# Performance work log

Measured on AMD Instinct MI355X. Metric: run time of the kernel, lower is better.

## Reference

```python
import jax, jax.numpy as jnp
import numpy as np

B, N, E = 64, 2048, 32768
F_IN, NHID, RULES = 256, 512, 128
RATIO = 0.5
K1 = int(np.ceil(RATIO * N)); K2 = int(np.ceil(RATIO * K1)); K3 = int(np.ceil(RATIO * K2))


def _gcn(x, src, dst, em, W, b):
    # GCNConv with self-loops and symmetric normalization; em is a float edge-validity mask.
    n = x.shape[0]
    h = x @ W  # [n, out]
    deg = jax.ops.segment_sum(em, dst, num_segments=n) + 1.0  # in-degree + self-loop
    dinv = jax.lax.rsqrt(deg)
    coef = dinv[src] * dinv[dst] * em  # [E]
    agg = jax.ops.segment_sum(h[src] * coef[:, None], dst, num_segments=n)
    return agg + h / deg[:, None] + b  # second term = self-loop with norm 1/deg


def _sag_pool(x, src, dst, em, Wg, bg, k):
    # SAGPooling: GCN scorer, per-graph top-k, scale kept nodes by tanh(score), filter+reindex edges.
    n = x.shape[0]
    score = _gcn(x, src, dst, em, Wg, bg)[:, 0]  # [n]
    vals, perm = jax.lax.top_k(score, k)
    xk = x[perm] * jnp.tanh(vals)[:, None]  # [k, F]
    newidx = jnp.full((n,), -1, dtype=src.dtype).at[perm].set(jnp.arange(k, dtype=src.dtype))
    ns, nd = newidx[src], newidx[dst]
    keep = em * (ns >= 0).astype(em.dtype) * (nd >= 0).astype(em.dtype)
    return xk, jnp.maximum(ns, 0), jnp.maximum(nd, 0), keep


_gcn_b = jax.vmap(_gcn, in_axes=(0, 0, 0, 0, None, None))
_pool_b = jax.vmap(_sag_pool, in_axes=(0, 0, 0, 0, None, None, None))


def setup_inputs() -> dict:
    key = jax.random.key(0)
    ks = jax.random.split(key, 16)
    def w(k, shape, fan_in):
        return jax.random.normal(k, shape, jnp.float32) * (1.0 / np.sqrt(fan_in))
    return {
        "x": jax.random.normal(ks[0], (B, N, F_IN), jnp.float32),
        "src": jax.random.randint(ks[1], (B, E), 0, N, jnp.int32),
        "dst": jax.random.randint(ks[2], (B, E), 0, N, jnp.int32),
        "W1": w(ks[3], (F_IN, NHID), F_IN), "b1": jnp.zeros((NHID,), jnp.float32),
        "Wp1": w(ks[4], (NHID, 1), NHID), "bp1": jnp.zeros((1,), jnp.float32),
        "W2": w(ks[5], (NHID, NHID), NHID), "b2": jnp.zeros((NHID,), jnp.float32),
        "Wp2": w(ks[6], (NHID, 1), NHID), "bp2": jnp.zeros((1,), jnp.float32),
        "W3": w(ks[7], (NHID, NHID), NHID), "b3": jnp.zeros((NHID,), jnp.float32),
        "Wp3": w(ks[8], (NHID, 1), NHID), "bp3": jnp.zeros((1,), jnp.float32),
        "lin1_W": w(ks[9], (2 * NHID, NHID), 2 * NHID), "lin1_b": jnp.zeros((NHID,), jnp.float32),
        "lin2_W": w(ks[10], (NHID, NHID // 2), NHID), "lin2_b": jnp.zeros((NHID // 2,), jnp.float32),
        "pi_W": w(ks[11], (NHID // 2, RULES), NHID // 2), "pi_b": jnp.zeros((RULES,), jnp.float32),
        "v_W": w(ks[12], (NHID // 2, 1), NHID // 2), "v_b": jnp.zeros((1,), jnp.float32),
    }


def reference(x, src, dst, W1, b1, Wp1, bp1, W2, b2, Wp2, bp2, W3, b3, Wp3, bp3,
              lin1_W, lin1_b, lin2_W, lin2_b, pi_W, pi_b, v_W, v_b):
    em = jnp.ones(src.shape, x.dtype)
    h = jax.nn.relu(_gcn_b(x, src, dst, em, W1, b1))
    h, s, d, em = _pool_b(h, src, dst, em, Wp1, bp1, K1)
    x1 = jnp.concatenate([h.max(axis=1), h.mean(axis=1)], axis=1)  # [B, 2*NHID]
    h = jax.nn.relu(_gcn_b(h, s, d, em, W2, b2))
    h, s, d, em = _pool_b(h, s, d, em, Wp2, bp2, K2)
    x2 = jnp.concatenate([h.max(axis=1), h.mean(axis=1)], axis=1)
    h = jax.nn.relu(_gcn_b(h, s, d, em, W3, b3))
    h, s, d, em = _pool_b(h, s, d, em, Wp3, bp3, K3)
    x3 = jnp.concatenate([h.max(axis=1), h.mean(axis=1)], axis=1)
    z = x1 + x2 + x3
    z = jax.nn.relu(z @ lin1_W + lin1_b)
    z = jax.nn.relu(z @ lin2_W + lin2_b)
    pi = jax.nn.log_softmax(z @ pi_W + pi_b, axis=1)
    v = jax.nn.relu(z @ v_W + v_b)
    return pi, v
```

## Files before the change

### kernel.cpp

```cpp
#include <hip/hip_runtime.h>
#include <math.h>
#include <cstdint>

#define B_   64
#define N_   2048
#define E_   32768
#define FIN  256
#define H_   512

typedef __bf16 bf16x8 __attribute__((ext_vector_type(8)));
typedef float  f32x4  __attribute__((ext_vector_type(4)));

__device__ __forceinline__ unsigned short f2bf(float f) {
  unsigned u = __float_as_uint(f);
  u += 0x7FFF + ((u >> 16) & 1);
  return (unsigned short)(u >> 16);
}
__device__ __forceinline__ unsigned pk2(float a, float b) {
  return (unsigned)f2bf(a) | ((unsigned)f2bf(b) << 16);
}
__device__ __forceinline__ float bflo(unsigned u) { return __uint_as_float(u << 16); }
__device__ __forceinline__ float bfhi(unsigned u) { return __uint_as_float(u & 0xFFFF0000u); }

__device__ __forceinline__ void accum8(float* acc, uint4 u, float c) {
  acc[0] += c * bflo(u.x); acc[1] += c * bfhi(u.x);
  acc[2] += c * bflo(u.y); acc[3] += c * bfhi(u.y);
  acc[4] += c * bflo(u.z); acc[5] += c * bfhi(u.z);
  acc[6] += c * bflo(u.w); acc[7] += c * bfhi(u.w);
}

__device__ __forceinline__ void glds16(const void* g, void* l) {
  __builtin_amdgcn_global_load_lds(
      (const __attribute__((address_space(1))) unsigned int*)g,
      (__attribute__((address_space(3))) unsigned int*)l, 16, 0, 0);
}

__global__ void xcvt_k(const float* __restrict__ x, unsigned short* __restrict__ xb) {
  int i = blockIdx.x * 256 + threadIdx.x;
  float4 f = reinterpret_cast<const float4*>(x)[i];
  uint2 o; o.x = pk2(f.x, f.y); o.y = pk2(f.z, f.w);
  reinterpret_cast<uint2*>(xb)[i] = o;
}

__global__ void wcvt_k(const float* __restrict__ W, unsigned short* __restrict__ Wt, int K) {
  int idx = blockIdx.x * 256 + threadIdx.x;
  int k = idx >> 9, n = idx & 511;
  Wt[n * K + k] = f2bf(W[idx]);
}

__global__ __launch_bounds__(256) void gemm_mfma(
    const unsigned short* __restrict__ Xb,
    const int* __restrict__ perm, const float* __restrict__ tanhv,
    const unsigned short* __restrict__ Wt, unsigned short* __restrict__ Y,
    int K, int kl2, int nsl2,
    const float* __restrict__ bias, const float* __restrict__ wp, float* __restrict__ hs) {
  __shared__ uint4 As[512];
  __shared__ uint4 Bs[512];
  const int tid = threadIdx.x;
  const int w = tid >> 6, L = tid & 63;
  const int bid = blockIdx.x;
  const int xcd = bid & 7;
  const int t = bid >> 3;
  const int colb = t & 3;
  const int strip = ((t >> 2) << 3) + xcd;
  const int m0 = strip * 128;
  const int n0 = colb * 128;
  const int e = L & 15, q = L >> 4;

  const int sw3 = (L >> 3) & 7;
  const int cA = (w * 64 + L) ^ sw3;
  const int rloc = cA >> 2;
  const int kcs = (cA & 3) * 8;

  f32x4 acc[4][4];
#pragma unroll
  for (int j = 0; j < 4; j++)
#pragma unroll
    for (int nn = 0; nn < 4; nn++) acc[j][nn] = (f32x4){0.f, 0.f, 0.f, 0.f};

  size_t asrc[2];
#pragma unroll
  for (int i = 0; i < 2; i++) {
    int g = m0 + i * 64 + rloc;
    size_t row;
    if (perm) {
      int b = g >> kl2;
      int node = perm[g];
      row = (size_t)(b << nsl2) + node;
    } else {
      row = (size_t)g;
    }
    asrc[i] = row * (size_t)K + kcs;
  }
  size_t bsrc[2];
#pragma unroll
  for (int i = 0; i < 2; i++) bsrc[i] = (size_t)(n0 + i * 64 + rloc) * K + kcs;

  const int fo = e * 4 + q;
  const int fosw = fo ^ (fo >> 3);

  for (int k0 = 0; k0 < K; k0 += 32) {
    glds16(Xb + asrc[0] + k0, &As[0 * 256 + w * 64]);
    glds16(Xb + asrc[1] + k0, &As[1 * 256 + w * 64]);
    glds16(Wt + bsrc[0] + k0, &Bs[0 * 256 + w * 64]);
    glds16(Wt + bsrc[1] + k0, &Bs[1 * 256 + w * 64]);
    __syncthreads();
    bf16x8 af[4], bfr[4];
#pragma unroll
    for (int j = 0; j < 4; j++) af[j]  = __builtin_bit_cast(bf16x8, As[((w & 1) * 4 + j) * 64 + fosw]);
#pragma unroll
    for (int j = 0; j < 4; j++) bfr[j] = __builtin_bit_cast(bf16x8, Bs[((w >> 1) * 4 + j) * 64 + fosw]);
#pragma unroll
    for (int j = 0; j < 4; j++)
#pragma unroll
      for (int nn = 0; nn < 4; nn++)
        acc[j][nn] = __builtin_amdgcn_mfma_f32_16x16x32_bf16(af[j], bfr[nn], acc[j][nn], 0, 0, 0);
    __syncthreads();
  }
  float bs[4], wsv[4];
#pragma unroll
  for (int nn = 0; nn < 4; nn++) {
    int coly = n0 + ((w >> 1) * 4 + nn) * 16 + e;
    bs[nn]  = bias ? bias[coly] : 0.f;
    wsv[nn] = wp ? wp[coly] : 0.f;
  }
#pragma unroll
  for (int j = 0; j < 4; j++) {
    int mt = (w & 1) * 4 + j;
#pragma unroll
    for (int r = 0; r < 4; r++) {
      int grow = m0 + mt * 16 + q * 4 + r;
      float t2 = tanhv ? tanhv[grow] : 1.0f;
      float p = 0.f;
#pragma unroll
      for (int nn = 0; nn < 4; nn++) {
        int coly = n0 + ((w >> 1) * 4 + nn) * 16 + e;
        float v = acc[j][nn][r] * t2;
        if (bias) v = fmaxf(v + bs[nn], 0.f);
        Y[(size_t)grow * 512 + coly] = f2bf(v);
        p += v * wsv[nn];
      }
      if (wp) {
        p += __shfl_xor(p, 1, 64); p += __shfl_xor(p, 2, 64);
        p += __shfl_xor(p, 4, 64); p += __shfl_xor(p, 8, 64);
        if ((L & 15) == 0) atomicAdd(&hs[grow], p);
      }
    }
  }
}

__global__ void count_k(const int* __restrict__ dst, int* __restrict__ cnt, int nl2) {
  int g = blockIdx.x * 256 + threadIdx.x;
  int d = dst[g];
  if (d < 0) return;
  int b = g >> 15;
  atomicAdd(&cnt[(b << nl2) + d], 1);
}

__global__ __launch_bounds__(256) void scan_k(const int* __restrict__ cnt,
                                              int* __restrict__ rowptr, int* __restrict__ cursor,
                                              float* __restrict__ deg, float* __restrict__ dinv, int n) {
  int b = blockIdx.x, tid = threadIdx.x;
  __shared__ int ls[2048];
  __shared__ int ch[256];
  int per = n >> 8;
  int base = tid * per;
  int s = 0;
  for (int i = 0; i < per; i++) { int v = cnt[b * n + base + i]; ls[base + i] = v; s += v; }
  ch[tid] = s;
  __syncthreads();
  for (int off = 1; off < 256; off <<= 1) {
    int v = (tid >= off) ? ch[tid - off] : 0;
    __syncthreads();
    ch[tid] += v;
    __syncthreads();
  }
  int run = (tid == 0) ? 0 : ch[tid - 1];
  for (int i = 0; i < per; i++) {
    int v = ls[base + i];
    rowptr[b * (n + 1) + base + i] = run;
    cursor[b * n + base + i] = run;
    float d = (float)(v + 1);
    deg[b * n + base + i] = d;
    dinv[b * n + base + i] = 1.0f / sqrtf(d);
    run += v;
  }
  if (tid == 255) rowptr[b * (n + 1) + n] = run;
}

__global__ void fill_k(const int* __restrict__ src, const int* __restrict__ dst,
                       const float* __restrict__ dinv, int* cursor, int* col,
                       float* ce, int nl2) {
  int g = blockIdx.x * 256 + threadIdx.x;
  int d = dst[g];
  if (d < 0) return;
  int b = g >> 15;
  int s = src[g];
  int pos = atomicAdd(&cursor[(b << nl2) + d], 1);
  col[(b << 15) + pos] = s;
  ce[(b << 15) + pos] = dinv[(b << nl2) + s] * dinv[(b << nl2) + d];
}

__global__ __launch_bounds__(256) void aggx_k(
    const unsigned short* __restrict__ X,
    const int* __restrict__ rowptr, const int* __restrict__ col,
    const float* __restrict__ ce, const float* __restrict__ deg,
    unsigned short* __restrict__ Xa) {
  const int w = threadIdx.x >> 6, L = threadIdx.x & 63;
  const int xcd = blockIdx.x & 7;
  const int slot = blockIdx.x >> 3;
  const int gslot = slot >> 9;
  const int v4 = slot & 511;
  const int b = (gslot << 3) + xcd;
  const int v = v4 * 4 + w;
  const int bbase = b << 11;
  const int vg = bbase + v;
  const int rb = b * (N_ + 1) + v;
  const int st = rowptr[rb], en = rowptr[rb + 1];
  const int* cb = col + (b << 15);
  const float* cee = ce + (b << 15);
  const int h = L >> 5, hl = L & 31;
  const unsigned short* Xb_ = X + (size_t)bbase * 256 + hl * 8;
  const int T = en - st + 1;
  const float selfc = 1.0f / deg[vg];
  float acc[8] = {0.f, 0.f, 0.f, 0.f, 0.f, 0.f, 0.f, 0.f};
  for (int t = h; t < T; t += 2) {
    bool isE = (t < T - 1);
    int s = isE ? cb[st + t] : v;
    float c = isE ? cee[st + t] : selfc;
    uint4 u = *(const uint4*)(Xb_ + (size_t)s * 256);
    accum8(acc, u, c);
  }
#pragma unroll
  for (int i = 0; i < 8; i++) acc[i] += __shfl_xor(acc[i], 32, 64);
  if (h == 0) {
    uint4 o;
    o.x = pk2(acc[0], acc[1]); o.y = pk2(acc[2], acc[3]);
    o.z = pk2(acc[4], acc[5]); o.w = pk2(acc[6], acc[7]);
    *(uint4*)(Xa + (size_t)vg * 256 + hl * 8) = o;
  }
}

template <int NL2>
__global__ __launch_bounds__(256) void agg_k(
    const unsigned short* __restrict__ H,
    const int* __restrict__ rowptr, const int* __restrict__ col,
    const float* __restrict__ ce, const float* __restrict__ deg,
    const float* __restrict__ bias, const float* __restrict__ wp,
    unsigned short* __restrict__ C, float* __restrict__ hs) {
  const int n = 1 << NL2;
  const int xcd = blockIdx.x & 7;
  const int slot = blockIdx.x >> 3;
  const int gslot = slot >> (NL2 - 2);
  const int v4 = slot & ((1 << (NL2 - 2)) - 1);
  const int b = (gslot << 3) + xcd;
  const int w = threadIdx.x >> 6, L = threadIdx.x & 63;
  const int v = v4 * 4 + w;
  const int bbase = b << NL2;
  const int vg = bbase + v;
  const int rb = b * (n + 1) + v;
  const int st = rowptr[rb], en = rowptr[rb + 1];
  const int* cb = col + (b << 15);
  const float* cee = ce + (b << 15);
  const unsigned short* Hb_ = H + (size_t)bbase * 512 + (size_t)L * 8;

  float acc[8] = {0.f, 0.f, 0.f, 0.f, 0.f, 0.f, 0.f, 0.f};
  int e2 = st;
  for (; e2 + 4 <= en; e2 += 4) {
    int s0 = cb[e2], s1 = cb[e2 + 1], s2 = cb[e2 + 2], s3 = cb[e2 + 3];
    float c0 = cee[e2], c1 = cee[e2 + 1], c2 = cee[e2 + 2], c3 = cee[e2 + 3];
    uint4 u0 = *(const uint4*)(Hb_ + (size_t)s0 * 512);
    uint4 u1 = *(const uint4*)(Hb_ + (size_t)s1 * 512);
    uint4 u2 = *(const uint4*)(Hb_ + (size_t)s2 * 512);
    uint4 u3 = *(const uint4*)(Hb_ + (size_t)s3 * 512);
    accum8(acc, u0, c0); accum8(acc, u1, c1);
    accum8(acc, u2, c2); accum8(acc, u3, c3);
  }
  for (; e2 < en; e2++) {
    int s = cb[e2];
    uint4 u = *(const uint4*)(Hb_ + (size_t)s * 512);
    accum8(acc, u, cee[e2]);
  }
  {
    float idg = 1.0f / deg[vg];
    uint4 u = *(const uint4*)(Hb_ + (size_t)v * 512);
    accum8(acc, u, idg);
  }
  float4 bLo = *(const float4*)(bias + L * 8);
  float4 bHi = *(const float4*)(bias + L * 8 + 4);
  acc[0] = fmaxf(acc[0] + bLo.x, 0.f); acc[1] = fmaxf(acc[1] + bLo.y, 0.f);
  acc[2] = fmaxf(acc[2] + bLo.z, 0.f); acc[3] = fmaxf(acc[3] + bLo.w, 0.f);
  acc[4] = fmaxf(acc[4] + bHi.x, 0.f); acc[5] = fmaxf(acc[5] + bHi.y, 0.f);
  acc[6] = fmaxf(acc[6] + bHi.z, 0.f); acc[7] = fmaxf(acc[7] + bHi.w, 0.f);
  uint4 o;
  o.x = pk2(acc[0], acc[1]); o.y = pk2(acc[2], acc[3]);
  o.z = pk2(acc[4], acc[5]); o.w = pk2(acc[6], acc[7]);
  *(uint4*)(C + (size_t)vg * 512 + L * 8) = o;
  float4 wLo = *(const float4*)(wp + L * 8);
  float4 wHi = *(const float4*)(wp + L * 8 + 4);
  float p = acc[0] * wLo.x + acc[1] * wLo.y + acc[2] * wLo.z + acc[3] * wLo.w
          + acc[4] * wHi.x + acc[5] * wHi.y + acc[6] * wHi.z + acc[7] * wHi.w;
#pragma unroll
  for (int off = 32; off > 0; off >>= 1) p += __shfl_down(p, off, 64);
  if (L == 0) hs[vg] = p;
}

__global__ void scoreagg_k(const float* __restrict__ hs, const int* __restrict__ rowptr,
                           const int* __restrict__ col, const float* __restrict__ ce,
                           const float* __restrict__ deg, const float* __restrict__ bp,
                           float* __restrict__ score, int nl2) {
  int idx = blockIdx.x * 256 + threadIdx.x;
  int n = 1 << nl2;
  int b = idx >> nl2, v = idx & (n - 1);
  int rb = b * (n + 1) + v;
  int st = rowptr[rb], en = rowptr[rb + 1];
  const int* cb = col + (b << 15);
  const float* cee = ce + (b << 15);
  int bbase = b << nl2;
  float acc = 0.f;
  int e = st;
  for (; e + 4 <= en; e += 4) {
    acc += hs[bbase + cb[e]] * cee[e] + hs[bbase + cb[e + 1]] * cee[e + 1]
         + hs[bbase + cb[e + 2]] * cee[e + 2] + hs[bbase + cb[e + 3]] * cee[e + 3];
  }
  for (; e < en; e++) acc += hs[bbase + cb[e]] * cee[e];
  score[idx] = acc + hs[idx] / deg[idx] + bp[0];
}

__global__ __launch_bounds__(1024) void topk_k(const float* __restrict__ score, int* __restrict__ perm,
                                               float* __restrict__ tanhv, int* __restrict__ newidx,
                                               int n, int k) {
  int b = blockIdx.x, tid = threadIdx.x;
  __shared__ float ss[2048];
  __shared__ int si[2048];
  for (int i = tid; i < n; i += 1024) { ss[i] = score[b * n + i]; si[i] = i; }
  __syncthreads();
  for (int size = 2; size <= n; size <<= 1) {
    for (int stride = size >> 1; stride > 0; stride >>= 1) {
      for (int i = tid; i < n; i += 1024) {
        int j = i ^ stride;
        if (j > i) {
          bool up = ((i & size) == 0);
          float fi = ss[i], fj = ss[j];
          int ii = si[i], ij = si[j];
          bool iBefore = (fi > fj) || (fi == fj && ii < ij);
          bool sw = up ? (!iBefore) : iBefore;
          if (sw) { ss[i] = fj; ss[j] = fi; si[i] = ij; si[j] = ii; }
        }
      }
      __syncthreads();
    }
  }
  for (int r = tid; r < n; r += 1024) newidx[b * n + si[r]] = (r < k) ? r : -1;
  for (int r = tid; r < k; r += 1024) { perm[b * k + r] = si[r]; tanhv[b * k + r] = tanhf(ss[r]); }
}

__global__ void reindex_count_k(const int* srcO, const int* dstO, const int* newidx,
                                int* srcN, int* dstN, int* cnt, int nl2new) {
  int g = blockIdx.x * 256 + threadIdx.x;
  int b = g >> 15;
  int dd = dstO[g];
  int sN = 0, dN = -1;
  if (dd >= 0) {
    int ns = newidx[(b << (nl2new + 1)) + srcO[g]];
    int nd = newidx[(b << (nl2new + 1)) + dd];
    if (ns >= 0 && nd >= 0) {
      sN = ns; dN = nd;
      atomicAdd(&cnt[(b << nl2new) + nd], 1);
    }
  }
  srcN[g] = sN; dstN[g] = dN;
}

__global__ __launch_bounds__(512) void statsp_k(const unsigned short* __restrict__ C,
    const int* __restrict__ perm, const float* __restrict__ tv,
    float* __restrict__ zp, int nsl2, int k, int kch) {
  int b = blockIdx.x, rg = blockIdx.y, f = threadIdx.x;
  int r0 = rg * kch;
  float mx = -1e30f, sm = 0.f;
#pragma unroll 4
  for (int r = r0; r < r0 + kch; r++) {
    int node = perm[b * k + r];
    float t = tv[b * k + r];
    float val = __uint_as_float((unsigned)C[((size_t)((b << nsl2) + node)) * 512 + f] << 16) * t;
    mx = fmaxf(mx, val); sm += val;
  }
  zp[(size_t)(b * 8 + rg) * 1024 + f] = mx;
  zp[(size_t)(b * 8 + rg) * 1024 + 512 + f] = sm;
}

__global__ __launch_bounds__(512) void statsr_k(const float* __restrict__ zp,
                                                float* __restrict__ z, int k) {
  int b = blockIdx.x, f = threadIdx.x;
  float mx = -1e30f, sm = 0.f;
#pragma unroll
  for (int g = 0; g < 8; g++) {
    mx = fmaxf(mx, zp[(size_t)(b * 8 + g) * 1024 + f]);
    sm += zp[(size_t)(b * 8 + g) * 1024 + 512 + f];
  }
  z[b * 1024 + f] += mx;
  z[b * 1024 + 512 + f] += sm / (float)k;
}

__global__ __launch_bounds__(256) void mlp_k(const float* __restrict__ z, const float* __restrict__ W1,
                                             const float* __restrict__ b1, const float* __restrict__ W2,
                                             const float* __restrict__ b2, const float* __restrict__ piW,
                                             const float* __restrict__ pib, const float* __restrict__ vW,
                                             const float* __restrict__ vb, float* __restrict__ out) {
  int b = blockIdx.x, tid = threadIdx.x;
  __shared__ float zr[1024];
  __shared__ float z1[512];
  __shared__ float z2[256];
  __shared__ float pl[128];
  __shared__ float red[2];
  for (int i = tid; i < 1024; i += 256) zr[i] = z[b * 1024 + i];
  __syncthreads();
  for (int o = tid; o < 512; o += 256) {
    float a = b1[o];
    for (int i = 0; i < 1024; i++) a += zr[i] * W1[i * 512 + o];
    z1[o] = fmaxf(a, 0.f);
  }
  __syncthreads();
  {
    int o = tid;
    float a = b2[o];
    for (int i = 0; i < 512; i++) a += z1[i] * W2[i * 256 + o];
    z2[o] = fmaxf(a, 0.f);
  }
  __syncthreads();
  if (tid < 128) {
    float a = pib[tid];
    for (int i = 0; i < 256; i++) a += z2[i] * piW[i * 128 + tid];
    pl[tid] = a;
  }
  __syncthreads();
  if (tid == 0) {
    float m = -1e30f;
    for (int i = 0; i < 128; i++) m = fmaxf(m, pl[i]);
    float se = 0.f;
    for (int i = 0; i < 128; i++) se += expf(pl[i] - m);
    red[0] = m; red[1] = logf(se);
    float a = vb[0];
    for (int i = 0; i < 256; i++) a += z2[i] * vW[i];
    out[B_ * 128 + b] = fmaxf(a, 0.f);
  }
  __syncthreads();
  if (tid < 128) out[b * 128 + tid] = pl[tid] - red[0] - red[1];
}

extern "C" void kernel_launch(void* const* d_in, const int* in_sizes, int n_in,
                              void* d_out, int out_size, void* d_ws, size_t ws_size,
                              hipStream_t stream) {
  const float* x    = (const float*)d_in[0];
  const int*   src0 = (const int*)d_in[1];
  const int*   dst0 = (const int*)d_in[2];
  const float* W1   = (const float*)d_in[3];
  const float* b1   = (const float*)d_in[4];
  const float* Wp1  = (const float*)d_in[5];
  const float* bp1  = (const float*)d_in[6];
  const float* W2   = (const float*)d_in[7];
  const float* b2   = (const float*)d_in[8];
  const float* Wp2  = (const float*)d_in[9];
  const float* bp2  = (const float*)d_in[10];
  const float* W3   = (const float*)d_in[11];
  const float* b3   = (const float*)d_in[12];
  const float* Wp3  = (const float*)d_in[13];
  const float* bp3  = (const float*)d_in[14];
  const float* l1W  = (const float*)d_in[15];
  const float* l1b  = (const float*)d_in[16];
  const float* l2W  = (const float*)d_in[17];
  const float* l2b  = (const float*)d_in[18];
  const float* piW  = (const float*)d_in[19];
  const float* pib  = (const float*)d_in[20];
  const float* vW   = (const float*)d_in[21];
  const float* vb   = (const float*)d_in[22];
  float* out = (float*)d_out;
  (void)in_sizes; (void)n_in; (void)out_size; (void)ws_size;

  unsigned short* Cb = (unsigned short*)d_in[0];

  char* base = (char*)d_ws;
  size_t off = 0;
  auto alloc = [&](size_t bytes) -> void* {
    void* r = base + off;
    off += (bytes + 255) & ~(size_t)255;
    return r;
  };
  unsigned short* Hb   = (unsigned short*)alloc((size_t)B_ * 1024 * H_ * 2);
  unsigned short* xb   = (unsigned short*)alloc((size_t)B_ * N_ * FIN * 2);
  unsigned short* Xa   = (unsigned short*)alloc((size_t)B_ * N_ * FIN * 2);
  unsigned short* W1t  = (unsigned short*)alloc((size_t)512 * 256 * 2);
  unsigned short* W2t  = (unsigned short*)alloc((size_t)512 * 512 * 2);
  unsigned short* W3t  = (unsigned short*)alloc((size_t)512 * 512 * 2);
  int*   srcA   = (int*)alloc((size_t)B_ * E_ * 4);
  int*   dstA   = (int*)alloc((size_t)B_ * E_ * 4);
  int*   col    = (int*)alloc((size_t)B_ * E_ * 4);
  float* coefE  = (float*)alloc((size_t)B_ * E_ * 4);
  int*   cnt    = (int*)alloc((size_t)B_ * N_ * 4);
  int*   cursor = (int*)alloc((size_t)B_ * N_ * 4);
  int*   rowptr = (int*)alloc((size_t)B_ * (N_ + 1) * 4);
  float* deg    = (float*)alloc((size_t)B_ * N_ * 4);
  float* dinv   = (float*)alloc((size_t)B_ * N_ * 4);
  float* hs     = (float*)alloc((size_t)B_ * N_ * 4);
  float* score  = (float*)alloc((size_t)B_ * N_ * 4);
  int*   newidx = (int*)alloc((size_t)B_ * N_ * 4);
  int*   perm   = (int*)alloc((size_t)B_ * 1024 * 4);
  float* tanhv  = (float*)alloc((size_t)B_ * 1024 * 4);
  float* zpart  = (float*)alloc((size_t)B_ * 8 * 1024 * 4);
  float* z      = (float*)alloc((size_t)B_ * 1024 * 4);

  const int EB = B_ * E_ / 256;

  xcvt_k<<<B_ * N_ * FIN / 4 / 256, 256, 0, stream>>>(x, xb);
  wcvt_k<<<256 * 512 / 256, 256, 0, stream>>>(W1, W1t, 256);
  wcvt_k<<<512 * 512 / 256, 256, 0, stream>>>(W2, W2t, 512);
  wcvt_k<<<512 * 512 / 256, 256, 0, stream>>>(W3, W3t, 512);
  hipMemsetAsync(z, 0, (size_t)B_ * 1024 * 4, stream);

  {
    hipMemsetAsync(cnt, 0, (size_t)B_ * 2048 * 4, stream);
    count_k<<<EB, 256, 0, stream>>>(dst0, cnt, 11);
    scan_k<<<B_, 256, 0, stream>>>(cnt, rowptr, cursor, deg, dinv, 2048);
    fill_k<<<EB, 256, 0, stream>>>(src0, dst0, dinv, cursor, col, coefE, 11);
    aggx_k<<<B_ * 2048 / 4, 256, 0, stream>>>(xb, rowptr, col, coefE, deg, Xa);
    hipMemsetAsync(hs, 0, (size_t)B_ * 2048 * 4, stream);
    gemm_mfma<<<B_ * 2048 / 128 * 4, 256, 0, stream>>>(
        Xa, nullptr, nullptr, W1t, Cb, 256, 0, 0, b1, Wp1, hs);
    scoreagg_k<<<B_ * 2048 / 256, 256, 0, stream>>>(hs, rowptr, col, coefE, deg, bp1, score, 11);
    topk_k<<<B_, 1024, 0, stream>>>(score, perm, tanhv, newidx, 2048, 1024);
    statsp_k<<<dim3(B_, 8), 512, 0, stream>>>(Cb, perm, tanhv, zpart, 11, 1024, 128);
    statsr_k<<<B_, 512, 0, stream>>>(zpart, z, 1024);
    hipMemsetAsync(cnt, 0, (size_t)B_ * 1024 * 4, stream);
    reindex_count_k<<<EB, 256, 0, stream>>>(src0, dst0, newidx, srcA, dstA, cnt, 10);
    scan_k<<<B_, 256, 0, stream>>>(cnt, rowptr, cursor, deg, dinv, 1024);
    fill_k<<<EB, 256, 0, stream>>>(srcA, dstA, dinv, cursor, col, coefE, 10);
  }
  {
    gemm_mfma<<<B_ * 1024 / 128 * 4, 256, 0, stream>>>(
        Cb, perm, tanhv, W2t, Hb, 512, 10, 11, nullptr, nullptr, nullptr);
    agg_k<10><<<B_ * 1024 / 4, 256, 0, stream>>>(Hb, rowptr, col, coefE, deg, b2, Wp2, Cb, hs);
    scoreagg_k<<<B_ * 1024 / 256, 256, 0, stream>>>(hs, rowptr, col, coefE, deg, bp2, score, 10);
    topk_k<<<B_, 1024, 0, stream>>>(score, perm, tanhv, newidx, 1024, 512);
    statsp_k<<<dim3(B_, 8), 512, 0, stream>>>(Cb, perm, tanhv, zpart, 10, 512, 64);
    statsr_k<<<B_, 512, 0, stream>>>(zpart, z, 512);
    hipMemsetAsync(cnt, 0, (size_t)B_ * 512 * 4, stream);
    reindex_count_k<<<EB, 256, 0, stream>>>(srcA, dstA, newidx, srcA, dstA, cnt, 9);
    scan_k<<<B_, 256, 0, stream>>>(cnt, rowptr, cursor, deg, dinv, 512);
    fill_k<<<EB, 256, 0, stream>>>(srcA, dstA, dinv, cursor, col, coefE, 9);
  }
  {
    gemm_mfma<<<B_ * 512 / 128 * 4, 256, 0, stream>>>(
        Cb, perm, tanhv, W3t, Hb, 512, 9, 10, nullptr, nullptr, nullptr);
    agg_k<9><<<B_ * 512 / 4, 256, 0, stream>>>(Hb, rowptr, col, coefE, deg, b3, Wp3, Cb, hs);
    scoreagg_k<<<B_ * 512 / 256, 256, 0, stream>>>(hs, rowptr, col, coefE, deg, bp3, score, 9);
    topk_k<<<B_, 1024, 0, stream>>>(score, perm, tanhv, newidx, 512, 256);
    statsp_k<<<dim3(B_, 8), 512, 0, stream>>>(Cb, perm, tanhv, zpart, 9, 256, 32);
    statsr_k<<<B_, 512, 0, stream>>>(zpart, z, 256);
  }

  mlp_k<<<B_, 256, 0, stream>>>(z, l1W, l1b, l2W, l2b, piW, pib, vW, vb, out);
}
```

Baseline: 1.104 ms.

## Widen GEMM tile to 128x256 with shuffle-packed vector stores and hardware bf16 pack

The MFMA GEMM tile grows from 128x128 to 128x256 outputs per block, so each wave holds a 4x8 accumulator grid and the A tile is reused across twice as many columns. Grid size is halved. The epilogue uses lane shuffles to pack neighbouring bf16 outputs into 8-byte stores instead of scalar 2-byte stores. On gfx950 the float-to-bf16 pack uses the native v_cvt_pk_bf16_f32 instruction. The trade-off is more registers and shared memory per block and fewer blocks, which may lower occupancy and wave parallelism on the smaller layer-3 GEMM.

New measurement: 1.256 ms. 1.14x slower.

```diff
diff --git a/kernel.cpp b/kernel.cpp
--- a/kernel.cpp
+++ b/kernel.cpp
@@ -17,7 +17,13 @@
   return (unsigned short)(u >> 16);
 }
 __device__ __forceinline__ unsigned pk2(float a, float b) {
+#if defined(__gfx950__)
+  unsigned r;
+  asm("v_cvt_pk_bf16_f32 %0, %1, %2" : "=v"(r) : "v"(a), "v"(b));
+  return r;
+#else
   return (unsigned)f2bf(a) | ((unsigned)f2bf(b) << 16);
+#endif
 }
 __device__ __forceinline__ float bflo(unsigned u) { return __uint_as_float(u << 16); }
 __device__ __forceinline__ float bfhi(unsigned u) { return __uint_as_float(u & 0xFFFF0000u); }
@@ -55,28 +61,28 @@
     int K, int kl2, int nsl2,
     const float* __restrict__ bias, const float* __restrict__ wp, float* __restrict__ hs) {
   __shared__ uint4 As[512];
-  __shared__ uint4 Bs[512];
+  __shared__ uint4 Bs[1024];
   const int tid = threadIdx.x;
   const int w = tid >> 6, L = tid & 63;
   const int bid = blockIdx.x;
   const int xcd = bid & 7;
   const int t = bid >> 3;
-  const int colb = t & 3;
-  const int strip = ((t >> 2) << 3) + xcd;
+  const int colb = t & 1;
+  const int strip = ((t >> 1) << 3) + xcd;
   const int m0 = strip * 128;
-  const int n0 = colb * 128;
   const int e = L & 15, q = L >> 4;
+  const int mh = w & 1, nh = w >> 1;
 
   const int sw3 = (L >> 3) & 7;
   const int cA = (w * 64 + L) ^ sw3;
   const int rloc = cA >> 2;
   const int kcs = (cA & 3) * 8;
 
-  f32x4 acc[4][4];
+  f32x4 acc[4][8];
 #pragma unroll
   for (int j = 0; j < 4; j++)
 #pragma unroll
-    for (int nn = 0; nn < 4; nn++) acc[j][nn] = (f32x4){0.f, 0.f, 0.f, 0.f};
+    for (int nn = 0; nn < 8; nn++) acc[j][nn] = (f32x4){0.f, 0.f, 0.f, 0.f};
 
   size_t asrc[2];
 #pragma unroll
@@ -92,9 +98,9 @@
     }
     asrc[i] = row * (size_t)K + kcs;
   }
-  size_t bsrc[2];
-#pragma unroll
-  for (int i = 0; i < 2; i++) bsrc[i] = (size_t)(n0 + i * 64 + rloc) * K + kcs;
+  size_t bsrc[4];
+#pragma unroll
+  for (int i = 0; i < 4; i++) bsrc[i] = (size_t)(colb * 256 + i * 64 + rloc) * K + kcs;
 
   const int fo = e * 4 + q;
   const int fosw = fo ^ (fo >> 3);
@@ -104,43 +110,69 @@
     glds16(Xb + asrc[1] + k0, &As[1 * 256 + w * 64]);
     glds16(Wt + bsrc[0] + k0, &Bs[0 * 256 + w * 64]);
     glds16(Wt + bsrc[1] + k0, &Bs[1 * 256 + w * 64]);
+    glds16(Wt + bsrc[2] + k0, &Bs[2 * 256 + w * 64]);
+    glds16(Wt + bsrc[3] + k0, &Bs[3 * 256 + w * 64]);
     __syncthreads();
-    bf16x8 af[4], bfr[4];
-#pragma unroll
-    for (int j = 0; j < 4; j++) af[j]  = __builtin_bit_cast(bf16x8, As[((w & 1) * 4 + j) * 64 + fosw]);
-#pragma unroll
-    for (int j = 0; j < 4; j++) bfr[j] = __builtin_bit_cast(bf16x8, Bs[((w >> 1) * 4 + j) * 64 + fosw]);
+    bf16x8 af[4], bfr[8];
 #pragma unroll
     for (int j = 0; j < 4; j++)
-#pragma unroll
-      for (int nn = 0; nn < 4; nn++)
+      af[j] = __builtin_bit_cast(bf16x8, As[mh * 256 + j * 64 + fosw]);
+#pragma unroll
+    for (int nn = 0; nn < 8; nn++)
+      bfr[nn] = __builtin_bit_cast(bf16x8, Bs[(nh * 2 + (nn >> 2)) * 256 + (nn & 3) * 64 + fosw]);
+#pragma unroll
+    for (int j = 0; j < 4; j++)
+#pragma unroll
+      for (int nn = 0; nn < 8; nn++)
         acc[j][nn] = __builtin_amdgcn_mfma_f32_16x16x32_bf16(af[j], bfr[nn], acc[j][nn], 0, 0, 0);
     __syncthreads();
   }
-  float bs[4], wsv[4];
-#pragma unroll
-  for (int nn = 0; nn < 4; nn++) {
-    int coly = n0 + ((w >> 1) * 4 + nn) * 16 + e;
+  const int colbase = colb * 256 + nh * 128;
+  float bs[8], wsv[8];
+#pragma unroll
+  for (int nn = 0; nn < 8; nn++) {
+    int coly = colbase + nn * 16 + e;
     bs[nn]  = bias ? bias[coly] : 0.f;
     wsv[nn] = wp ? wp[coly] : 0.f;
   }
 #pragma unroll
   for (int j = 0; j < 4; j++) {
-    int mt = (w & 1) * 4 + j;
 #pragma unroll
     for (int r = 0; r < 4; r++) {
-      int grow = m0 + mt * 16 + q * 4 + r;
+      int grow = m0 + (mh * 4 + j) * 16 + q * 4 + r;
       float t2 = tanhv ? tanhv[grow] : 1.0f;
-      float p = 0.f;
-#pragma unroll
-      for (int nn = 0; nn < 4; nn++) {
-        int coly = n0 + ((w >> 1) * 4 + nn) * 16 + e;
-        float v = acc[j][nn][r] * t2;
-        if (bias) v = fmaxf(v + bs[nn], 0.f);
-        Y[(size_t)grow * 512 + coly] = f2bf(v);
-        p += v * wsv[nn];
+      float v[8];
+#pragma unroll
+      for (int nn = 0; nn < 8; nn++) {
+        float val = acc[j][nn][r] * t2;
+        if (bias) val = fmaxf(val + bs[nn], 0.f);
+        v[nn] = val;
+      }
+      unsigned u[4];
+      const bool odd = (e & 1);
+#pragma unroll
+      for (int tt = 0; tt < 4; tt++) {
+        float a = v[2 * tt], b = v[2 * tt + 1];
+        float a2 = __shfl_xor(a, 1, 64);
+        float b2 = __shfl_xor(b, 1, 64);
+        u[tt] = odd ? pk2(b2, b) : pk2(a, a2);
+      }
+      unsigned short* Yr = Y + (size_t)grow * 512;
+#pragma unroll
+      for (int s = 0; s < 2; s++) {
+        unsigned ua = u[2 * s], ub = u[2 * s + 1];
+        unsigned ua2 = __shfl_xor(ua, 2, 64);
+        unsigned ub2 = __shfl_xor(ub, 2, 64);
+        uint2 wv;
+        if (e & 2) { wv.x = ub2; wv.y = ub; }
+        else       { wv.x = ua;  wv.y = ua2; }
+        int T = s * 4 + (e & 3);
+        *(uint2*)(Yr + colbase + T * 16 + (e & 12)) = wv;
       }
       if (wp) {
+        float p = 0.f;
+#pragma unroll
+        for (int nn = 0; nn < 8; nn++) p += v[nn] * wsv[nn];
         p += __shfl_xor(p, 1, 64); p += __shfl_xor(p, 2, 64);
         p += __shfl_xor(p, 4, 64); p += __shfl_xor(p, 8, 64);
         if ((L & 15) == 0) atomicAdd(&hs[grow], p);
@@ -524,7 +556,7 @@
     fill_k<<<EB, 256, 0, stream>>>(src0, dst0, dinv, cursor, col, coefE, 11);
     aggx_k<<<B_ * 2048 / 4, 256, 0, stream>>>(xb, rowptr, col, coefE, deg, Xa);
     hipMemsetAsync(hs, 0, (size_t)B_ * 2048 * 4, stream);
-    gemm_mfma<<<B_ * 2048 / 128 * 4, 256, 0, stream>>>(
+    gemm_mfma<<<B_ * 2048 / 128 * 2, 256, 0, stream>>>(
         Xa, nullptr, nullptr, W1t, Cb, 256, 0, 0, b1, Wp1, hs);
     scoreagg_k<<<B_ * 2048 / 256, 256, 0, stream>>>(hs, rowptr, col, coefE, deg, bp1, score, 11);
     topk_k<<<B_, 1024, 0, stream>>>(score, perm, tanhv, newidx, 2048, 1024);
@@ -536,7 +568,7 @@
     fill_k<<<EB, 256, 0, stream>>>(srcA, dstA, dinv, cursor, col, coefE, 10);
   }
   {
-    gemm_mfma<<<B_ * 1024 / 128 * 4, 256, 0, stream>>>(
+    gemm_mfma<<<B_ * 1024 / 128 * 2, 256, 0, stream>>>(
         Cb, perm, tanhv, W2t, Hb, 512, 10, 11, nullptr, nullptr, nullptr);
     agg_k<10><<<B_ * 1024 / 4, 256, 0, stream>>>(Hb, rowptr, col, coefE, deg, b2, Wp2, Cb, hs);
     scoreagg_k<<<B_ * 1024 / 256, 256, 0, stream>>>(hs, rowptr, col, coefE, deg, bp2, score, 10);
@@ -549,7 +581,7 @@
     fill_k<<<EB, 256, 0, stream>>>(srcA, dstA, dinv, cursor, col, coefE, 9);
   }
   {
-    gemm_mfma<<<B_ * 512 / 128 * 4, 256, 0, stream>>>(
+    gemm_mfma<<<B_ * 512 / 128 * 2, 256, 0, stream>>>(
         Cb, perm, tanhv, W3t, Hb, 512, 9, 10, nullptr, nullptr, nullptr);
     agg_k<9><<<B_ * 512 / 4, 256, 0, stream>>>(Hb, rowptr, col, coefE, deg, b3, Wp3, Cb, hs);
     scoreagg_k<<<B_ * 512 / 256, 256, 0, stream>>>(hs, rowptr, col, coefE, deg, bp3, score, 9);
```
